# Kernel tuning notes

Measured on AMD Instinct MI355X. Metric: run time of the kernel, lower is better.

The kernel has to match this reference:

```python
import jax, jax.numpy as jnp
import numpy as np
import math

D_MODEL = 512
N_HEADS = 8
D_K = D_MODEL // N_HEADS
BS, N_EDGES, N_NODES = 4, 1024, 4096


def setup_inputs() -> dict:
    key = jax.random.key(0)
    ks = jax.random.split(key, 12)
    s = 1.0 / math.sqrt(D_MODEL)
    return {
        "queries": jax.random.normal(ks[0], (BS, N_EDGES, D_MODEL), jnp.float32),
        "keys": jax.random.normal(ks[1], (BS, N_NODES, D_MODEL), jnp.float32),
        "incidence_matrix": jax.random.randint(ks[2], (BS, N_EDGES, N_NODES), 0, 2, jnp.int32),
        "Wq": jax.random.normal(ks[3], (D_MODEL, D_MODEL), jnp.float32) * s,
        "bq": jax.random.normal(ks[4], (D_MODEL,), jnp.float32) * s,
        "Wk": jax.random.normal(ks[5], (D_MODEL, D_MODEL), jnp.float32) * s,
        "bk": jax.random.normal(ks[6], (D_MODEL,), jnp.float32) * s,
        "Wv": jax.random.normal(ks[7], (D_MODEL, D_MODEL), jnp.float32) * s,
        "bv": jax.random.normal(ks[8], (D_MODEL,), jnp.float32) * s,
        "Wo": jax.random.normal(ks[9], (D_MODEL, D_MODEL), jnp.float32) * s,
        "bo": jax.random.normal(ks[10], (D_MODEL,), jnp.float32) * s,
    }


def reference(queries, keys, incidence_matrix, Wq, bq, Wk, bk, Wv, bv, Wo, bo):
    bs, E, _ = queries.shape
    N = keys.shape[1]
    # QKV projections (torch Linear: x @ W.T + b), split heads -> (bs, H, len, d_k)
    Q = (queries @ Wq.T + bq).reshape(bs, E, N_HEADS, D_K).transpose(0, 2, 1, 3)
    K = (keys @ Wk.T + bk).reshape(bs, N, N_HEADS, D_K).transpose(0, 2, 1, 3)
    V = (keys @ Wv.T + bv).reshape(bs, N, N_HEADS, D_K).transpose(0, 2, 1, 3)
    # scores: (bs, H, E, N)
    scores = jnp.einsum("bhed,bhnd->bhen", Q, K) / math.sqrt(D_K)
    mask = (incidence_matrix == 0)[:, None, :, :]  # (bs, 1, E, N)
    scores = jnp.where(mask, jnp.float32(-1e9), scores)
    attn = jax.nn.softmax(scores, axis=-1)
    # dropout is identity in eval mode
    out = jnp.einsum("bhen,bhnd->bhed", attn, V)  # (bs, H, E, d_k)
    out = out.transpose(0, 2, 1, 3).reshape(bs, E, D_MODEL)
    return out @ Wo.T + bo
```

## Files before the change

kernel.cpp:

```cpp
#include <hip/hip_runtime.h>

#define DMODEL 512
#define NHEADS 8
#define DK 64
#define BSZ 4
#define NE 1024
#define NNODE 4096

typedef __attribute__((ext_vector_type(8))) __bf16 bf16x8;
typedef __attribute__((ext_vector_type(4))) float f32x4;
typedef __attribute__((ext_vector_type(8))) unsigned short u16x8;
typedef __attribute__((ext_vector_type(4))) unsigned short u16x4;

static __device__ __forceinline__ unsigned short f2bf(float f) {
    union { float f; unsigned int u; } v; v.f = f;
    unsigned int u = v.u;
    return (unsigned short)((u + 0x7FFFu + ((u >> 16) & 1u)) >> 16);
}

static __device__ __forceinline__ unsigned cvtpk(float lo, float hi) {
    unsigned r;
    asm("v_cvt_pk_bf16_f32 %0, %1, %2" : "=v"(r) : "v"(lo), "v"(hi));
    return r;
}

static __device__ __forceinline__ bf16x8 ldb8(const unsigned short* p) {
    return *reinterpret_cast<const bf16x8*>(p);
}

static __device__ __forceinline__ void gload16(const unsigned short* g,
                                               unsigned short* l) {
    __builtin_amdgcn_global_load_lds(
        (const __attribute__((address_space(1))) unsigned int*)g,
        (__attribute__((address_space(3))) unsigned int*)l, 16, 0, 0);
}

__global__ __launch_bounds__(256) void convk(const float4* __restrict__ src,
                                             u16x8* __restrict__ dst) {
    int i = blockIdx.x * 256 + threadIdx.x;
    float4 a = src[2 * i];
    float4 b = src[2 * i + 1];
    unsigned u0 = cvtpk(a.x, a.y), u1 = cvtpk(a.z, a.w);
    unsigned u2 = cvtpk(b.x, b.y), u3 = cvtpk(b.z, b.w);
    u16x8 o;
    o[0] = (unsigned short)u0; o[1] = (unsigned short)(u0 >> 16);
    o[2] = (unsigned short)u1; o[3] = (unsigned short)(u1 >> 16);
    o[4] = (unsigned short)u2; o[5] = (unsigned short)(u2 >> 16);
    o[6] = (unsigned short)u3; o[7] = (unsigned short)(u3 >> 16);
    dst[i] = o;
}

__global__ __launch_bounds__(256) void convw4(const float4* __restrict__ a,
                                              const float4* __restrict__ b,
                                              const float4* __restrict__ c,
                                              const float4* __restrict__ d,
                                              u16x8* __restrict__ dst) {
    int i = blockIdx.x * 256 + threadIdx.x;
    int sel = i >> 15;
    const float4* s = sel == 0 ? a : sel == 1 ? b : sel == 2 ? c : d;
    int j = i & 32767;
    float4 x = s[2 * j];
    float4 y = s[2 * j + 1];
    unsigned u0 = cvtpk(x.x, x.y), u1 = cvtpk(x.z, x.w);
    unsigned u2 = cvtpk(y.x, y.y), u3 = cvtpk(y.z, y.w);
    u16x8 o;
    o[0] = (unsigned short)u0; o[1] = (unsigned short)(u0 >> 16);
    o[2] = (unsigned short)u1; o[3] = (unsigned short)(u1 >> 16);
    o[4] = (unsigned short)u2; o[5] = (unsigned short)(u2 >> 16);
    o[6] = (unsigned short)u3; o[7] = (unsigned short)(u3 >> 16);
    dst[i] = o;
}

__global__ __launch_bounds__(256) void maskpack(const int* __restrict__ inc,
                                                unsigned long long* __restrict__ mb) {
    int wid = blockIdx.x * 4 + (threadIdx.x >> 6);
    int lane = threadIdx.x & 63;
#pragma unroll
    for (int j = 0; j < 8; ++j) {
        int g = wid * 8 + j;
        int v = inc[(size_t)g * 64 + lane];
        unsigned long long m = __ballot(v != 0);
        if (lane == 0) mb[g] = m;
    }
}

template <int MODE>
__global__ __launch_bounds__(256) void gemm128(const unsigned short* __restrict__ A,
                                               const unsigned short* __restrict__ W,
                                               const float* __restrict__ bias,
                                               void* __restrict__ Cout, float oscale) {
    int w = threadIdx.x >> 6, l = threadIdx.x & 63;
    int lr = l & 15, lh = l >> 4;
    int wm = w >> 1, wn = w & 1;
    int m0 = blockIdx.x * 128, n0 = blockIdx.y * 128;

    __shared__ unsigned short Ast[2][128][64];
    __shared__ unsigned short Bst[2][128][64];

    int srow = w * 32 + (l >> 3);
    int scu = l & 7;

    auto stage = [&](int bf, int k0) {
#pragma unroll
        for (int ii = 0; ii < 4; ++ii) {
            int row = srow + ii * 8;
            int cu = scu ^ (row & 7);
            gload16(A + (size_t)(m0 + row) * DMODEL + k0 + cu * 8,
                    &Ast[bf][w * 32 + ii * 8][0]);
            gload16(W + (size_t)(n0 + row) * DMODEL + k0 + cu * 8,
                    &Bst[bf][w * 32 + ii * 8][0]);
        }
    };

    f32x4 acc[4][4] = {};

    stage(0, 0);
    __syncthreads();

    int bf = 0;
    for (int t = 0; t < 8; ++t) {
        if (t < 7) stage(bf ^ 1, (t + 1) * 64);
#pragma unroll
        for (int half = 0; half < 2; ++half) {
            bf16x8 af[4], bfr[4];
#pragma unroll
            for (int mf = 0; mf < 4; ++mf)
                af[mf] = ldb8(&Ast[bf][wm * 64 + mf * 16 + lr]
                                  [((half * 4 + lh) ^ (lr & 7)) * 8]);
#pragma unroll
            for (int nf = 0; nf < 4; ++nf)
                bfr[nf] = ldb8(&Bst[bf][wn * 64 + nf * 16 + lr]
                                   [((half * 4 + lh) ^ (lr & 7)) * 8]);
#pragma unroll
            for (int mf = 0; mf < 4; ++mf)
#pragma unroll
                for (int nf = 0; nf < 4; ++nf)
                    acc[mf][nf] = __builtin_amdgcn_mfma_f32_16x16x32_bf16(
                        af[mf], bfr[nf], acc[mf][nf], 0, 0, 0);
        }
        __syncthreads();
        bf ^= 1;
    }

    if constexpr (MODE == 0) {
        unsigned short* C = (unsigned short*)Cout;
#pragma unroll
        for (int nf = 0; nf < 4; ++nf) {
            int ncol = n0 + wn * 64 + nf * 16 + lr;
            float bv = bias[ncol];
#pragma unroll
            for (int mf = 0; mf < 4; ++mf)
#pragma unroll
                for (int r = 0; r < 4; ++r)
                    C[(size_t)(m0 + wm * 64 + mf * 16 + lh * 4 + r) * DMODEL + ncol] =
                        f2bf((acc[mf][nf][r] + bv) * oscale);
        }
    } else if constexpr (MODE == 1) {
        unsigned short* Vt = (unsigned short*)Cout;
        int bb = m0 >> 12;
        int nodebase = (m0 & (NNODE - 1)) + wm * 64;
#pragma unroll
        for (int nf = 0; nf < 4; ++nf) {
            int ncol = n0 + wn * 64 + nf * 16;
            int hh = ncol >> 6;
            int dd = (ncol & 63) + lr;
            float bv = bias[ncol + lr];
#pragma unroll
            for (int mf = 0; mf < 4; ++mf) {
                u16x4 pk;
#pragma unroll
                for (int r = 0; r < 4; ++r) pk[r] = f2bf(acc[mf][nf][r] + bv);
                int node0 = nodebase + mf * 16 + lh * 4;
                *reinterpret_cast<u16x4*>(
                    Vt + (size_t)((bb * NHEADS + hh) * DK + dd) * NNODE + node0) = pk;
            }
        }
    } else {
        float* C = (float*)Cout;
#pragma unroll
        for (int nf = 0; nf < 4; ++nf) {
            int ncol = n0 + wn * 64 + nf * 16 + lr;
            float bv = bias[ncol];
#pragma unroll
            for (int mf = 0; mf < 4; ++mf)
#pragma unroll
                for (int r = 0; r < 4; ++r)
                    C[(size_t)(m0 + wm * 64 + mf * 16 + lh * 4 + r) * DMODEL + ncol] =
                        acc[mf][nf][r] + bv;
        }
    }
}

__global__ __launch_bounds__(256) void attn_kernel(
    const unsigned short* __restrict__ Qb, const unsigned short* __restrict__ Kb,
    const unsigned short* __restrict__ Vt, const unsigned long long* __restrict__ mbits,
    unsigned short* __restrict__ Ob) {
    int w = threadIdx.x >> 6, l = threadIdx.x & 63;
    int lr = l & 15, lh = l >> 4;
    int id = blockIdx.x;
    int xcd = id & 7, et = (id >> 3) & 15, ps = id >> 7;
    int pair = xcd * 4 + ps;
    int b = pair >> 3, h = pair & 7;
    int e0 = et * 64 + w * 16;

    __shared__ unsigned short Kst[2][64][64];
    __shared__ unsigned short Vst[2][64][64];
    __shared__ unsigned short Pt[4][16][76];
    unsigned short* Pw = &Pt[w][0][0];

    const unsigned short* Qrow = Qb + (size_t)(b * NE + e0 + lr) * DMODEL + h * DK;
    bf16x8 q0 = ldb8(Qrow + lh * 8);
    bf16x8 q1 = ldb8(Qrow + 32 + lh * 8);

    const unsigned short* Kg = Kb + (size_t)b * NNODE * DMODEL + h * DK;
    const unsigned short* Vg = Vt + (size_t)((b * NHEADS + h) * DK) * NNODE;
    const unsigned long long* mrow = mbits + (size_t)(b * NE + e0) * 64;

    int srow0 = w * 16 + (l >> 3);
    int scol = l & 7;

    f32x4 oacc[4] = {};
    float lsum[4] = {0.f, 0.f, 0.f, 0.f};

    auto stage = [&](int bf, int cb) {
#pragma unroll
        for (int ii = 0; ii < 2; ++ii) {
            int row = srow0 + ii * 8;
            int cu = scol ^ (row & 7);
            gload16(Kg + (size_t)(cb * 64 + row) * DMODEL + cu * 8,
                    &Kst[bf][w * 16 + ii * 8][0]);
            gload16(Vg + (size_t)row * NNODE + cb * 64 + cu * 8,
                    &Vst[bf][w * 16 + ii * 8][0]);
        }
    };

    unsigned long long mcur[4], mnext[4];

    stage(0, 0);
#pragma unroll
    for (int r = 0; r < 4; ++r) mcur[r] = mrow[(lh * 4 + r) * 64];
    __syncthreads();

    int bf = 0;
    for (int cb = 0; cb < 64; ++cb) {
        if (cb < 63) {
            stage(bf ^ 1, cb + 1);
#pragma unroll
            for (int r = 0; r < 4; ++r) mnext[r] = mrow[(lh * 4 + r) * 64 + cb + 1];
        }
        bf16x8 kf[4][2];
#pragma unroll
        for (int t = 0; t < 4; ++t) {
            int row = t * 16 + lr;
            kf[t][0] = ldb8(&Kst[bf][row][((0 + lh) ^ (lr & 7)) * 8]);
            kf[t][1] = ldb8(&Kst[bf][row][((4 + lh) ^ (lr & 7)) * 8]);
        }
        f32x4 s[4] = {};
#pragma unroll
        for (int t = 0; t < 4; ++t) {
            s[t] = __builtin_amdgcn_mfma_f32_16x16x32_bf16(q0, kf[t][0], s[t], 0, 0, 0);
            s[t] = __builtin_amdgcn_mfma_f32_16x16x32_bf16(q1, kf[t][1], s[t], 0, 0, 0);
        }
        bf16x8 vf[2][4];
#pragma unroll
        for (int kk = 0; kk < 2; ++kk)
#pragma unroll
            for (int dt = 0; dt < 4; ++dt) {
                int row = dt * 16 + lr;
                vf[kk][dt] = ldb8(&Vst[bf][row][((kk * 4 + lh) ^ (lr & 7)) * 8]);
            }
#pragma unroll
        for (int t = 0; t < 4; ++t) {
#pragma unroll
            for (int r = 0; r < 4; ++r) {
                float p = __expf(s[t][r]);
                unsigned half = (t < 2) ? (unsigned)mcur[r] : (unsigned)(mcur[r] >> 32);
                unsigned bits = half >> ((t & 1) * 16 + lr);
                p = (bits & 1u) ? p : 0.0f;
                s[t][r] = p;
                lsum[r] += p;
            }
            unsigned p01 = cvtpk(s[t][0], s[t][1]);
            unsigned p23 = cvtpk(s[t][2], s[t][3]);
            Pw[(lh * 4 + 0) * 76 + t * 16 + lr] = (unsigned short)p01;
            Pw[(lh * 4 + 1) * 76 + t * 16 + lr] = (unsigned short)(p01 >> 16);
            Pw[(lh * 4 + 2) * 76 + t * 16 + lr] = (unsigned short)p23;
            Pw[(lh * 4 + 3) * 76 + t * 16 + lr] = (unsigned short)(p23 >> 16);
        }
#pragma unroll
        for (int kk = 0; kk < 2; ++kk) {
            bf16x8 pa = ldb8(Pw + lr * 76 + kk * 32 + lh * 8);
#pragma unroll
            for (int dt = 0; dt < 4; ++dt) {
                oacc[dt] = __builtin_amdgcn_mfma_f32_16x16x32_bf16(pa, vf[kk][dt],
                                                                   oacc[dt], 0, 0, 0);
            }
        }
        __syncthreads();
        bf ^= 1;
#pragma unroll
        for (int r = 0; r < 4; ++r) mcur[r] = mnext[r];
    }

#pragma unroll
    for (int r = 0; r < 4; ++r) {
        float v = lsum[r];
        v += __shfl_xor(v, 1);
        v += __shfl_xor(v, 2);
        v += __shfl_xor(v, 4);
        v += __shfl_xor(v, 8);
        lsum[r] = v;
    }
#pragma unroll
    for (int r = 0; r < 4; ++r) {
        float inv = 1.0f / lsum[r];
        size_t row = (size_t)(b * NE + e0 + lh * 4 + r) * DMODEL + h * DK;
#pragma unroll
        for (int dt = 0; dt < 4; ++dt) {
            Ob[row + dt * 16 + lr] = f2bf(oacc[dt][r] * inv);
        }
    }
}

extern "C" void kernel_launch(void* const* d_in, const int* in_sizes, int n_in,
                              void* d_out, int out_size, void* d_ws, size_t ws_size,
                              hipStream_t stream) {
    const float* queries = (const float*)d_in[0];
    const float* keys = (const float*)d_in[1];
    const int* inc = (const int*)d_in[2];
    const float* Wq = (const float*)d_in[3];
    const float* bq = (const float*)d_in[4];
    const float* Wk = (const float*)d_in[5];
    const float* bk = (const float*)d_in[6];
    const float* Wv = (const float*)d_in[7];
    const float* bv = (const float*)d_in[8];
    const float* Wo = (const float*)d_in[9];
    const float* bo = (const float*)d_in[10];

    unsigned long long* mbits = (unsigned long long*)d_ws;
    unsigned short* wqb = (unsigned short*)(mbits + BSZ * NE * 64);
    unsigned short* wkb = wqb + DMODEL * DMODEL;
    unsigned short* wvb = wkb + DMODEL * DMODEL;
    unsigned short* wob = wvb + DMODEL * DMODEL;
    unsigned short* qbf = wob + DMODEL * DMODEL;
    unsigned short* kbf = qbf + (size_t)BSZ * NE * DMODEL;
    unsigned short* Qb = kbf + (size_t)BSZ * NNODE * DMODEL;
    unsigned short* Kb = Qb + (size_t)BSZ * NE * DMODEL;
    unsigned short* Vt = Kb + (size_t)BSZ * NNODE * DMODEL;
    unsigned short* Ob = Vt + (size_t)BSZ * NNODE * DMODEL;

    convk<<<BSZ * NE * DMODEL / 8 / 256, 256, 0, stream>>>((const float4*)queries,
                                                           (u16x8*)qbf);
    convk<<<BSZ * NNODE * DMODEL / 8 / 256, 256, 0, stream>>>((const float4*)keys,
                                                              (u16x8*)kbf);
    convw4<<<512, 256, 0, stream>>>((const float4*)Wq, (const float4*)Wk,
                                    (const float4*)Wv, (const float4*)Wo, (u16x8*)wqb);
    maskpack<<<8192, 256, 0, stream>>>(inc, mbits);

    gemm128<0><<<dim3(BSZ * NE / 128, 4), 256, 0, stream>>>(qbf, wqb, bq, Qb, 0.125f);
    gemm128<0><<<dim3(BSZ * NNODE / 128, 4), 256, 0, stream>>>(kbf, wkb, bk, Kb, 1.0f);
    gemm128<1><<<dim3(BSZ * NNODE / 128, 4), 256, 0, stream>>>(kbf, wvb, bv, Vt, 1.0f);

    attn_kernel<<<dim3(512), 256, 0, stream>>>(Qb, Kb, Vt, mbits, Ob);

    gemm128<2><<<dim3(BSZ * NE / 128, 4), 256, 0, stream>>>(Ob, wob, bo, d_out, 1.0f);
}
```

Measured before the change: 328.5 us.

## Split attention over two node segments with combine pass, fuse conversions, use exp2

Splits the attention kernel's node loop into two halves processed by separate blocks (1024 blocks instead of 512), writing unnormalized fp32 partial outputs and row sums that a new combine kernel adds, normalizes and converts to bf16. This is meant to raise occupancy and parallelism on the many-CU GPU, at the cost of extra fp32 partial traffic and an extra launch. It also folds log2(e) into the Q scale so the softmax can use raw v_exp_f32, and merges the three conversion kernels into one launch. Workspace offsets are reorganized so the partial buffers reuse the qbf/kbf region after the projections.

```diff
diff --git a/kernel.cpp b/kernel.cpp
--- a/kernel.cpp
+++ b/kernel.cpp
@@ -24,6 +24,12 @@
     return r;
 }
 
+static __device__ __forceinline__ float exp2v(float x) {
+    float r;
+    asm("v_exp_f32 %0, %1" : "=v"(r) : "v"(x));
+    return r;
+}
+
 static __device__ __forceinline__ bf16x8 ldb8(const unsigned short* p) {
     return *reinterpret_cast<const bf16x8*>(p);
 }
@@ -35,30 +41,26 @@
         (__attribute__((address_space(3))) unsigned int*)l, 16, 0, 0);
 }
 
-__global__ __launch_bounds__(256) void convk(const float4* __restrict__ src,
-                                             u16x8* __restrict__ dst) {
+__global__ __launch_bounds__(256) void conv_all(
+    const float4* __restrict__ q, const float4* __restrict__ k,
+    const float4* __restrict__ wq, const float4* __restrict__ wk,
+    const float4* __restrict__ wv, const float4* __restrict__ wo,
+    u16x8* __restrict__ qb, u16x8* __restrict__ kb, u16x8* __restrict__ wb) {
     int i = blockIdx.x * 256 + threadIdx.x;
-    float4 a = src[2 * i];
-    float4 b = src[2 * i + 1];
-    unsigned u0 = cvtpk(a.x, a.y), u1 = cvtpk(a.z, a.w);
-    unsigned u2 = cvtpk(b.x, b.y), u3 = cvtpk(b.z, b.w);
-    u16x8 o;
-    o[0] = (unsigned short)u0; o[1] = (unsigned short)(u0 >> 16);
-    o[2] = (unsigned short)u1; o[3] = (unsigned short)(u1 >> 16);
-    o[4] = (unsigned short)u2; o[5] = (unsigned short)(u2 >> 16);
-    o[6] = (unsigned short)u3; o[7] = (unsigned short)(u3 >> 16);
-    dst[i] = o;
-}
-
-__global__ __launch_bounds__(256) void convw4(const float4* __restrict__ a,
-                                              const float4* __restrict__ b,
-                                              const float4* __restrict__ c,
-                                              const float4* __restrict__ d,
-                                              u16x8* __restrict__ dst) {
-    int i = blockIdx.x * 256 + threadIdx.x;
-    int sel = i >> 15;
-    const float4* s = sel == 0 ? a : sel == 1 ? b : sel == 2 ? c : d;
-    int j = i & 32767;
+    const float4* s;
+    u16x8* d;
+    int j;
+    if (i < 262144) {
+        s = q; d = qb; j = i;
+    } else if (i < 1310720) {
+        s = k; d = kb; j = i - 262144;
+    } else {
+        int t = i - 1310720;
+        int sel = t >> 15;
+        s = sel == 0 ? wq : sel == 1 ? wk : sel == 2 ? wv : wo;
+        d = wb + ((size_t)sel << 15);
+        j = t & 32767;
+    }
     float4 x = s[2 * j];
     float4 y = s[2 * j + 1];
     unsigned u0 = cvtpk(x.x, x.y), u1 = cvtpk(x.z, x.w);
@@ -68,7 +70,7 @@
     o[2] = (unsigned short)u1; o[3] = (unsigned short)(u1 >> 16);
     o[4] = (unsigned short)u2; o[5] = (unsigned short)(u2 >> 16);
     o[6] = (unsigned short)u3; o[7] = (unsigned short)(u3 >> 16);
-    dst[i] = o;
+    d[j] = o;
 }
 
 __global__ __launch_bounds__(256) void maskpack(const int* __restrict__ inc,
@@ -194,11 +196,13 @@
 __global__ __launch_bounds__(256) void attn_kernel(
     const unsigned short* __restrict__ Qb, const unsigned short* __restrict__ Kb,
     const unsigned short* __restrict__ Vt, const unsigned long long* __restrict__ mbits,
-    unsigned short* __restrict__ Ob) {
+    float* __restrict__ Op, float* __restrict__ Lp) {
     int w = threadIdx.x >> 6, l = threadIdx.x & 63;
     int lr = l & 15, lh = l >> 4;
     int id = blockIdx.x;
-    int xcd = id & 7, et = (id >> 3) & 15, ps = id >> 7;
+    int xcd = id & 7, et = (id >> 3) & 15;
+    int rest = id >> 7;
+    int ps = rest & 3, seg = rest >> 2;
     int pair = xcd * 4 + ps;
     int b = pair >> 3, h = pair & 7;
     int e0 = et * 64 + w * 16;
@@ -212,9 +216,11 @@
     bf16x8 q0 = ldb8(Qrow + lh * 8);
     bf16x8 q1 = ldb8(Qrow + 32 + lh * 8);
 
-    const unsigned short* Kg = Kb + (size_t)b * NNODE * DMODEL + h * DK;
-    const unsigned short* Vg = Vt + (size_t)((b * NHEADS + h) * DK) * NNODE;
-    const unsigned long long* mrow = mbits + (size_t)(b * NE + e0) * 64;
+    const unsigned short* Kg =
+        Kb + (size_t)(b * NNODE + seg * 2048) * DMODEL + h * DK;
+    const unsigned short* Vg =
+        Vt + (size_t)((b * NHEADS + h) * DK) * NNODE + seg * 2048;
+    const unsigned long long* mrow = mbits + (size_t)(b * NE + e0) * 64 + seg * 32;
 
     int srow0 = w * 16 + (l >> 3);
     int scol = l & 7;
@@ -242,8 +248,8 @@
     __syncthreads();
 
     int bf = 0;
-    for (int cb = 0; cb < 64; ++cb) {
-        if (cb < 63) {
+    for (int cb = 0; cb < 32; ++cb) {
+        if (cb < 31) {
             stage(bf ^ 1, cb + 1);
 #pragma unroll
             for (int r = 0; r < 4; ++r) mnext[r] = mrow[(lh * 4 + r) * 64 + cb + 1];
@@ -273,7 +279,7 @@
         for (int t = 0; t < 4; ++t) {
 #pragma unroll
             for (int r = 0; r < 4; ++r) {
-                float p = __expf(s[t][r]);
+                float p = exp2v(s[t][r]);
                 unsigned half = (t < 2) ? (unsigned)mcur[r] : (unsigned)(mcur[r] >> 32);
                 unsigned bits = half >> ((t & 1) * 16 + lr);
                 p = (bits & 1u) ? p : 0.0f;
@@ -311,15 +317,47 @@
         v += __shfl_xor(v, 8);
         lsum[r] = v;
     }
+    float* Opf = Op + (size_t)seg * (BSZ * NE * DMODEL);
+    float* Lpf = Lp + (size_t)seg * (BSZ * NHEADS * NE);
 #pragma unroll
     for (int r = 0; r < 4; ++r) {
-        float inv = 1.0f / lsum[r];
         size_t row = (size_t)(b * NE + e0 + lh * 4 + r) * DMODEL + h * DK;
 #pragma unroll
-        for (int dt = 0; dt < 4; ++dt) {
-            Ob[row + dt * 16 + lr] = f2bf(oacc[dt][r] * inv);
-        }
-    }
+        for (int dt = 0; dt < 4; ++dt) Opf[row + dt * 16 + lr] = oacc[dt][r];
+    }
+    if (lr == 0) {
+#pragma unroll
+        for (int r = 0; r < 4; ++r)
+            Lpf[(size_t)(b * NHEADS + h) * NE + e0 + lh * 4 + r] = lsum[r];
+    }
+}
+
+__global__ __launch_bounds__(256) void combine2(const float* __restrict__ O0,
+                                                const float* __restrict__ O1,
+                                                const float* __restrict__ L0,
+                                                const float* __restrict__ L1,
+                                                unsigned short* __restrict__ Ob) {
+    int gi = blockIdx.x * 256 + threadIdx.x;
+    size_t base = (size_t)gi * 8;
+    int row = (int)(base >> 9);
+    int h = ((int)base & 511) >> 6;
+    int b = row >> 10, e = row & 1023;
+    size_t li = (size_t)(b * NHEADS + h) * NE + e;
+    float inv = 1.0f / (L0[li] + L1[li]);
+    float4 a0 = *reinterpret_cast<const float4*>(O0 + base);
+    float4 a1 = *reinterpret_cast<const float4*>(O0 + base + 4);
+    float4 b0 = *reinterpret_cast<const float4*>(O1 + base);
+    float4 b1 = *reinterpret_cast<const float4*>(O1 + base + 4);
+    unsigned u0 = cvtpk((a0.x + b0.x) * inv, (a0.y + b0.y) * inv);
+    unsigned u1 = cvtpk((a0.z + b0.z) * inv, (a0.w + b0.w) * inv);
+    unsigned u2 = cvtpk((a1.x + b1.x) * inv, (a1.y + b1.y) * inv);
+    unsigned u3 = cvtpk((a1.z + b1.z) * inv, (a1.w + b1.w) * inv);
+    u16x8 o;
+    o[0] = (unsigned short)u0; o[1] = (unsigned short)(u0 >> 16);
+    o[2] = (unsigned short)u1; o[3] = (unsigned short)(u1 >> 16);
+    o[4] = (unsigned short)u2; o[5] = (unsigned short)(u2 >> 16);
+    o[6] = (unsigned short)u3; o[7] = (unsigned short)(u3 >> 16);
+    *reinterpret_cast<u16x8*>(Ob + base) = o;
 }
 
 extern "C" void kernel_launch(void* const* d_in, const int* in_sizes, int n_in,
@@ -337,31 +375,37 @@
     const float* Wo = (const float*)d_in[9];
     const float* bo = (const float*)d_in[10];
 
-    unsigned long long* mbits = (unsigned long long*)d_ws;
-    unsigned short* wqb = (unsigned short*)(mbits + BSZ * NE * 64);
+    char* base = (char*)d_ws;
+    unsigned long long* mbits = (unsigned long long*)base;
+    unsigned short* wqb = (unsigned short*)(base + (2u << 20));
+    unsigned short* qbf = (unsigned short*)(base + (4u << 20));
+    unsigned short* kbf = (unsigned short*)(base + (8u << 20));
+    unsigned short* Qb = (unsigned short*)(base + (24u << 20));
+    unsigned short* Kb = (unsigned short*)(base + (28u << 20));
+    unsigned short* Vt = (unsigned short*)(base + (44u << 20));
+    unsigned short* Ob = (unsigned short*)(base + (60u << 20));
+    float* Op0 = (float*)(base + (4u << 20));
+    float* Lp0 = (float*)(base + (20u << 20));
+
+    conv_all<<<5632, 256, 0, stream>>>((const float4*)queries, (const float4*)keys,
+                                       (const float4*)Wq, (const float4*)Wk,
+                                       (const float4*)Wv, (const float4*)Wo,
+                                       (u16x8*)qbf, (u16x8*)kbf, (u16x8*)wqb);
+    maskpack<<<8192, 256, 0, stream>>>(inc, mbits);
+
     unsigned short* wkb = wqb + DMODEL * DMODEL;
     unsigned short* wvb = wkb + DMODEL * DMODEL;
     unsigned short* wob = wvb + DMODEL * DMODEL;
-    unsigned short* qbf = wob + DMODEL * DMODEL;
-    unsigned short* kbf = qbf + (size_t)BSZ * NE * DMODEL;
-    unsigned short* Qb = kbf + (size_t)BSZ * NNODE * DMODEL;
-    unsigned short* Kb = Qb + (size_t)BSZ * NE * DMODEL;
-    unsigned short* Vt = Kb + (size_t)BSZ * NNODE * DMODEL;
-    unsigned short* Ob = Vt + (size_t)BSZ * NNODE * DMODEL;
-
-    convk<<<BSZ * NE * DMODEL / 8 / 256, 256, 0, stream>>>((const float4*)queries,
-                                                           (u16x8*)qbf);
-    convk<<<BSZ * NNODE * DMODEL / 8 / 256, 256, 0, stream>>>((const float4*)keys,
-                                                              (u16x8*)kbf);
-    convw4<<<512, 256, 0, stream>>>((const float4*)Wq, (const float4*)Wk,
-                                    (const float4*)Wv, (const float4*)Wo, (u16x8*)wqb);
-    maskpack<<<8192, 256, 0, stream>>>(inc, mbits);
-
-    gemm128<0><<<dim3(BSZ * NE / 128, 4), 256, 0, stream>>>(qbf, wqb, bq, Qb, 0.125f);
+
+    gemm128<0><<<dim3(BSZ * NE / 128, 4), 256, 0, stream>>>(qbf, wqb, bq, Qb,
+                                                            0.18033688f);
     gemm128<0><<<dim3(BSZ * NNODE / 128, 4), 256, 0, stream>>>(kbf, wkb, bk, Kb, 1.0f);
     gemm128<1><<<dim3(BSZ * NNODE / 128, 4), 256, 0, stream>>>(kbf, wvb, bv, Vt, 1.0f);
 
-    attn_kernel<<<dim3(512), 256, 0, stream>>>(Qb, Kb, Vt, mbits, Ob);
+    attn_kernel<<<dim3(1024), 256, 0, stream>>>(Qb, Kb, Vt, mbits, Op0, Lp0);
+
+    combine2<<<dim3(1024), 256, 0, stream>>>(Op0, Op0 + (size_t)BSZ * NE * DMODEL, Lp0,
+                                             Lp0 + (size_t)BSZ * NHEADS * NE, Ob);
 
     gemm128<2><<<dim3(BSZ * NE / 128, 4), 256, 0, stream>>>(Ob, wob, bo, d_out, 1.0f);
 }
```

Result: no change. 323.1 us (-1.6%).
